# Kernel tuning notes

Measured on AMD Instinct MI355X. Metric: run time of the kernel, lower is better.

## Reference

```python
import jax, jax.numpy as jnp
import numpy as np

BN_EPS = 1e-5


def _bn_relu(h, gamma, beta):
    # BatchNorm1d in training mode: batch stats over the edge dimension, biased var
    mu = jnp.mean(h, axis=0)
    var = jnp.mean((h - mu) ** 2, axis=0)
    return jax.nn.relu((h - mu) * jax.lax.rsqrt(var + BN_EPS) * gamma + beta)


def setup_inputs() -> dict:
    key = jax.random.key(0)
    ks = jax.random.split(key, 6)
    B, P, C, O, K = 8, 2048, 64, 64, 20  # clouds, points/cloud, in_ch, out_ch, knn
    N = B * P
    x = jax.random.normal(ks[0], (N, C), jnp.float32)
    pos = jax.random.normal(ks[1], (N, 3), jnp.float32)
    batch = jnp.repeat(jnp.arange(B, dtype=jnp.int32), P)  # sorted cloud ids
    # MLP params: Linear(2C, O) -> BN -> ReLU -> Linear(O, O) -> BN -> ReLU
    W1 = jax.random.normal(ks[2], (O, 2 * C), jnp.float32) / np.sqrt(2 * C)
    b1 = jnp.zeros((O,), jnp.float32)
    g1 = jnp.ones((O,), jnp.float32)
    beta1 = jnp.zeros((O,), jnp.float32)
    W2 = jax.random.normal(ks[3], (O, O), jnp.float32) / np.sqrt(O)
    b2 = jnp.zeros((O,), jnp.float32)
    g2 = jnp.ones((O,), jnp.float32)
    beta2 = jnp.zeros((O,), jnp.float32)
    return {"x": x, "pos": pos, "batch": batch, "W1": W1, "b1": b1, "g1": g1,
            "beta1": beta1, "W2": W2, "b2": b2, "g2": g2, "beta2": beta2, "k": K}


def reference(x, pos, batch, W1, b1, g1, beta1, W2, b2, g2, beta2, k):
    N, C = x.shape
    B = int(batch[-1]) + 1          # equal-size, sorted clouds
    P = N // B
    p = pos.reshape(B, P, -1)
    # knn_graph (loop=False): brute-force squared distances per cloud
    sq = jnp.sum(p * p, axis=-1)                      # [B,P]
    d2 = sq[:, :, None] + sq[:, None, :] - 2.0 * jnp.einsum('bpd,bqd->bpq', p, p)
    d2 = jnp.where(jnp.eye(P, dtype=bool)[None], jnp.inf, d2)  # no self-loops
    _, nbr = jax.lax.top_k(-d2, k)                    # [B,P,k] neighbor idx in cloud
    offset = (jnp.arange(B, dtype=nbr.dtype) * P)[:, None, None]
    # torch_cluster knn_graph flow='source_to_target': row = neighbor j, col = center i
    row = (nbr + offset).reshape(-1)                  # [N*k]
    col = jnp.repeat(jnp.arange(N, dtype=row.dtype), k)
    x_r = x[row]
    edge_features = jnp.concatenate([x_r, x[col] - x_r], axis=1)  # [N*k, 2C]
    h = _bn_relu(edge_features @ W1.T + b1, g1, beta1)
    h = _bn_relu(h @ W2.T + b2, g2, beta2)
    out = jax.ops.segment_max(h, row, num_segments=N)
    # torch_scatter scatter(reduce='max') leaves empty rows at 0
    return jnp.where(jnp.isneginf(out), 0.0, out)
```

## Files before the change

### kernel.cpp

```cpp
#include <hip/hip_runtime.h>

constexpr int BATCH = 8;
constexpr int PPC   = 2048;
constexpr int NPT   = BATCH * PPC;
constexpr int OCH   = 64;
constexpr int KNN_K = 20;
constexpr int NEDGE = NPT * KNN_K;
constexpr int REVCAP = 128;
constexpr int OVCAP  = 8192;
constexpr int QCAP   = 48;
constexpr int NPART  = 32;

typedef short short8 __attribute__((ext_vector_type(8)));
typedef float float4v __attribute__((ext_vector_type(4)));

__device__ __forceinline__ int xcd_swizzle(int b, int nper) {
  return (b & 7) * nper + (b >> 3);
}

__device__ __forceinline__ unsigned short bfr(float f) {
  unsigned u = __float_as_uint(f);
  return (unsigned short)((u + 0x7FFFu + ((u >> 16) & 1u)) >> 16);
}
__device__ __forceinline__ short8 pack8(float4 a, float4 b) {
  short8 r;
  r[0] = (short)bfr(a.x); r[1] = (short)bfr(a.y);
  r[2] = (short)bfr(a.z); r[3] = (short)bfr(a.w);
  r[4] = (short)bfr(b.x); r[5] = (short)bfr(b.y);
  r[6] = (short)bfr(b.z); r[7] = (short)bfr(b.w);
  return r;
}
__device__ __forceinline__ unsigned umed3(unsigned a, unsigned b, unsigned c) {
  unsigned d;
  asm("v_med3_u32 %0, %1, %2, %3" : "=v"(d) : "v"(a), "v"(b), "v"(c));
  return d;
}

__global__ __launch_bounds__(256) void knn_kernel(const float* __restrict__ pos,
                                                  int* __restrict__ nbr,
                                                  int* __restrict__ cnt,
                                                  int* __restrict__ ovf_cnt,
                                                  int* __restrict__ ovf,
                                                  int* __restrict__ rev) {
  __shared__ float4 cps[8 * 257];
  __shared__ unsigned long long qk[16][QCAP];
  __shared__ int qn[16];
  const int t  = threadIdx.x;
  const int pl = t >> 4;
  const int s  = t & 15;
  const int lane = t & 63;
  const int eb = xcd_swizzle(blockIdx.x, NPT / 16 / 8);
  const int i  = eb * 16 + pl;
  const int cbase = i & ~(PPC - 1);

  for (int u = t; u < PPC; u += 256) {
    int j = cbase + u;
    float ax = pos[3 * j], ay = pos[3 * j + 1], az = pos[3 * j + 2];
    cps[(u >> 8) * 257 + (u & 255)] = make_float4(ax, ay, az, ax * ax + ay * ay + az * az);
  }
  if (t < 16) qn[t] = 0;
  __syncthreads();

  const int il = i - cbase;
  const float4 me = cps[(il >> 8) * 257 + (il & 255)];
  const float px = me.x, py = me.y, pz = me.z, sqi = me.w;
  const int jbase = s * 128;
  const float4* __restrict__ cp = &cps[(s >> 1) * 257 + (s & 1) * 128];

  unsigned kd[3];
  kd[0] = kd[1] = kd[2] = 0xFFFFFFFFu;
  for (int u = 0; u < 128; ++u) {
    float4 c = cp[u];
    float pr = fmaf(-px, c.x, fmaf(-py, c.y, fmaf(-pz, c.z, fmaf(0.5f, c.w, 1000.f))));
    unsigned ck = __float_as_uint(pr);
    ck = (jbase + u == il) ? 0xFFFFFFFFu : ck;
    kd[2] = umed3(kd[1], kd[2], ck);
    kd[1] = umed3(kd[0], kd[1], ck);
    kd[0] = kd[0] < ck ? kd[0] : ck;
  }

  unsigned T = 0xFFFFFFFFu;
  int cum = 0;
  const int grp = lane & 48;
#pragma unroll
  for (int r = 0; r < KNN_K; ++r) {
    unsigned w = kd[0];
#pragma unroll
    for (int m = 1; m < 16; m <<= 1) {
      unsigned o = (unsigned)__shfl_xor((int)w, m, 16);
      w = o < w ? o : w;
    }
    bool pop = (kd[0] == w);
    unsigned long long bal = __ballot(pop);
    int mcount = __popc((int)((bal >> grp) & 0xFFFFull));
    if (cum < KNN_K) T = w;
    cum += mcount;
    if (pop) { kd[0] = kd[1]; kd[1] = kd[2]; kd[2] = 0xFFFFFFFFu; }
  }
  const unsigned Tq = T + 16;

  for (int u = 0; u < 128; ++u) {
    float4 c = cp[u];
    float pr = fmaf(-px, c.x, fmaf(-py, c.y, fmaf(-pz, c.z, fmaf(0.5f, c.w, 1000.f))));
    unsigned ck = __float_as_uint(pr);
    ck = (jbase + u == il) ? 0xFFFFFFFFu : ck;
    if (ck <= Tq) {
      float d2 = sqi + c.w - 2.0f * (px * c.x + py * c.y + pz * c.z);
      d2 = d2 > 0.f ? d2 : 0.f;
      int slot = atomicAdd(&qn[pl], 1);
      if (slot < QCAP)
        qk[pl][slot] = ((unsigned long long)__float_as_uint(d2) << 32) | (unsigned)(jbase + u);
    }
  }
  __syncthreads();

  int n = qn[pl]; n = n < QCAP ? n : QCAP;
  for (int base = 0; base < n; base += 16) {
    int e = base + s;
    if (e < n) {
      unsigned long long mk = qk[pl][e];
      int rank = 0;
      for (int o = 0; o < n; ++o) rank += (qk[pl][o] < mk) ? 1 : 0;
      if (rank < KNN_K) {
        int j = cbase + (int)(mk & 0xFFFFFFFFull);
        int eid = i * KNN_K + rank;
        nbr[eid] = j;
        int slot = atomicAdd(&cnt[j], 1);
        if (slot < REVCAP) rev[j * REVCAP + slot] = i;
        else { int ov = atomicAdd(ovf_cnt, 1); if (ov < OVCAP) ovf[ov] = eid; }
      }
    }
  }
}

__global__ __launch_bounds__(256) void node_gemm(const float* __restrict__ x,
                                                 const float* __restrict__ W1,
                                                 float* __restrict__ yv,
                                                 float* __restrict__ zv) {
  __shared__ float wa[64][65];
  __shared__ float wb[64][65];
  __shared__ float xs[16][64];
  const int t = threadIdx.x;
  for (int m = t; m < 8192; m += 256) {
    int o = m >> 7, c2 = m & 127;
    float w = W1[m];
    if (c2 < 64) wa[c2][o] = w; else wb[c2 - 64][o] = w;
  }
  for (int m = t; m < 1024; m += 256)
    xs[m >> 6][m & 63] = x[(size_t)blockIdx.x * 1024 + m];
  __syncthreads();
  const int g = t >> 6, o = t & 63;
  float accA[4] = {0, 0, 0, 0}, accB[4] = {0, 0, 0, 0};
#pragma unroll 4
  for (int c = 0; c < 64; ++c) {
    float w_a = wa[c][o], w_b = wb[c][o];
#pragma unroll
    for (int q = 0; q < 4; ++q) {
      float xv = xs[g * 4 + q][c];
      accA[q] = fmaf(xv, w_a, accA[q]);
      accB[q] = fmaf(xv, w_b, accB[q]);
    }
  }
#pragma unroll
  for (int q = 0; q < 4; ++q) {
    size_t n = (size_t)blockIdx.x * 16 + g * 4 + q;
    yv[n * 64 + o] = accA[q] - accB[q];
    zv[n * 64 + o] = accB[q];
  }
}

__global__ __launch_bounds__(256) void bn1_stats(const int* __restrict__ nbr,
                                                 const float4* __restrict__ yv4,
                                                 const float4* __restrict__ zv4,
                                                 const float* __restrict__ b1,
                                                 float* __restrict__ bn1p) {
  const int t  = threadIdx.x;
  const int c4 = t & 15;
  const int lane = t & 63;
  const int eb = xcd_swizzle(blockIdx.x, NPT / 16 / 8);
  const int i  = eb * 16 + (t >> 4);
  const float4 bo = reinterpret_cast<const float4*>(b1)[c4];
  float4 z = zv4[(size_t)i * 16 + c4];
  float4 zb = make_float4(z.x + bo.x, z.y + bo.y, z.z + bo.z, z.w + bo.w);
  int jA = nbr[i * KNN_K + c4];
  int jB = nbr[i * KNN_K + 16 + (c4 & 3)];
  float4 s1 = make_float4(0, 0, 0, 0), s2 = make_float4(0, 0, 0, 0);
#pragma unroll
  for (int q = 0; q < 16; ++q) {
    int j = __shfl(jA, (lane & 48) + q);
    float4 y = yv4[(size_t)j * 16 + c4];
    float sx = y.x + zb.x, sy = y.y + zb.y, sz = y.z + zb.z, sw = y.w + zb.w;
    s1.x += sx; s1.y += sy; s1.z += sz; s1.w += sw;
    s2.x += sx * sx; s2.y += sy * sy; s2.z += sz * sz; s2.w += sw * sw;
  }
#pragma unroll
  for (int q = 0; q < 4; ++q) {
    int j = __shfl(jB, (lane & 48) + q);
    float4 y = yv4[(size_t)j * 16 + c4];
    float sx = y.x + zb.x, sy = y.y + zb.y, sz = y.z + zb.z, sw = y.w + zb.w;
    s1.x += sx; s1.y += sy; s1.z += sz; s1.w += sw;
    s2.x += sx * sx; s2.y += sy * sy; s2.z += sz * sz; s2.w += sw * sw;
  }
  s1.x += __shfl_xor(s1.x, 16); s1.y += __shfl_xor(s1.y, 16);
  s1.z += __shfl_xor(s1.z, 16); s1.w += __shfl_xor(s1.w, 16);
  s2.x += __shfl_xor(s2.x, 16); s2.y += __shfl_xor(s2.y, 16);
  s2.z += __shfl_xor(s2.z, 16); s2.w += __shfl_xor(s2.w, 16);
  s1.x += __shfl_xor(s1.x, 32); s1.y += __shfl_xor(s1.y, 32);
  s1.z += __shfl_xor(s1.z, 32); s1.w += __shfl_xor(s1.w, 32);
  s2.x += __shfl_xor(s2.x, 32); s2.y += __shfl_xor(s2.y, 32);
  s2.z += __shfl_xor(s2.z, 32); s2.w += __shfl_xor(s2.w, 32);
  __shared__ float ss[2][64];
  if (t < 128) { ss[0][t & 63] = 0.f; }
  __syncthreads();
  if ((t & 48) == 0) {
    atomicAdd(&ss[0][c4 * 4 + 0], s1.x); atomicAdd(&ss[0][c4 * 4 + 1], s1.y);
    atomicAdd(&ss[0][c4 * 4 + 2], s1.z); atomicAdd(&ss[0][c4 * 4 + 3], s1.w);
    atomicAdd(&ss[1][c4 * 4 + 0], s2.x); atomicAdd(&ss[1][c4 * 4 + 1], s2.y);
    atomicAdd(&ss[1][c4 * 4 + 2], s2.z); atomicAdd(&ss[1][c4 * 4 + 3], s2.w);
  }
  __syncthreads();
  const int pb = (blockIdx.x & (NPART - 1)) * 128;
  if (t < 64)       atomicAdd(&bn1p[pb + t], ss[0][t]);
  else if (t < 128) atomicAdd(&bn1p[pb + 64 + (t - 64)], ss[1][t - 64]);
}

__global__ __launch_bounds__(256) void scale_yz(
    const float4* __restrict__ yv4, const float4* __restrict__ zv4,
    const float* __restrict__ bn1p, const float* __restrict__ g1,
    const float* __restrict__ beta1, const float* __restrict__ b1,
    float4* __restrict__ ys4, float4* __restrict__ zs4) {
  __shared__ float red[128];
  const int t = threadIdx.x;
  if (t < 128) {
    float v = 0.f;
#pragma unroll
    for (int k = 0; k < NPART; ++k) v += bn1p[k * 128 + t];
    red[t] = v;
  }
  __syncthreads();
  const int idx = blockIdx.x * 256 + t;
  const int c4 = idx & 15;
  constexpr float invE = 1.0f / NEDGE;
  float a[4], c[4];
#pragma unroll
  for (int q = 0; q < 4; ++q) {
    int ch = c4 * 4 + q;
    float mu  = red[ch] * invE;
    float var = red[64 + ch] * invE - mu * mu;
    float av  = g1[ch] * rsqrtf(var + 1e-5f);
    a[q] = av;
    c[q] = fmaf(b1[ch], av, beta1[ch] - mu * av);
  }
  float4 y = yv4[idx];
  float4 z = zv4[idx];
  ys4[idx] = make_float4(y.x * a[0], y.y * a[1], y.z * a[2], y.w * a[3]);
  zs4[idx] = make_float4(fmaf(z.x, a[0], c[0]), fmaf(z.y, a[1], c[1]),
                         fmaf(z.z, a[2], c[2]), fmaf(z.w, a[3], c[3]));
}

__global__ __launch_bounds__(256) void gemm2_row(
    const float4* __restrict__ ys4, const float4* __restrict__ zs4,
    const float* __restrict__ W2, const float* __restrict__ b2,
    const int* __restrict__ cnt, const int* __restrict__ rev,
    float* __restrict__ bn2p, float* __restrict__ mmax,
    float* __restrict__ mmin) {
  __shared__ float ss[2][64];
  const int t = threadIdx.x, lane = t & 63;
  const int col = lane & 15, quad = lane >> 4;
  const int eb = xcd_swizzle(blockIdx.x, NPT / 16 / 8);
  const int wid = eb * 4 + (t >> 6);

  short8 bf0[4], bf1[4];
  const float4* __restrict__ W2v = (const float4*)W2;
#pragma unroll
  for (int nt = 0; nt < 4; ++nt) {
    int row = nt * 16 + col;
    float4 wa = W2v[row * 16 + quad * 2];
    float4 wb = W2v[row * 16 + quad * 2 + 1];
    float4 wc = W2v[row * 16 + 8 + quad * 2];
    float4 wd = W2v[row * 16 + 8 + quad * 2 + 1];
    bf0[nt] = pack8(wa, wb);
    bf1[nt] = pack8(wc, wd);
  }
  float b2r[4];
#pragma unroll
  for (int nt = 0; nt < 4; ++nt) b2r[nt] = b2[nt * 16 + col];

  int4 cq = *reinterpret_cast<const int4*>(&cnt[wid * 4]);
  int nA[4] = {cq.x, cq.y, cq.z, cq.w};
#pragma unroll
  for (int q = 0; q < 4; ++q) nA[q] = nA[q] < REVCAP ? nA[q] : REVCAP;

  float s1[4] = {0, 0, 0, 0}, s2[4] = {0, 0, 0, 0};
  int rv0 = rev[(size_t)(wid * 4) * REVCAP + lane];
  int rv1 = (nA[0] > 64) ? rev[(size_t)(wid * 4) * REVCAP + 64 + lane] : 0;
  float4 ya = ys4[(size_t)(wid * 4) * 16 + quad * 2];
  float4 yb = ys4[(size_t)(wid * 4) * 16 + quad * 2 + 1];
  float4 yc = ys4[(size_t)(wid * 4) * 16 + 8 + quad * 2];
  float4 yd = ys4[(size_t)(wid * 4) * 16 + 8 + quad * 2 + 1];

#pragma unroll
  for (int rr = 0; rr < 4; ++rr) {
    const int row = wid * 4 + rr;
    const int n = nA[rr];
    int nrv0 = 0, nrv1 = 0;
    float4 nya, nyb, nyc, nyd;
    if (rr < 3) {
      const int nrow = row + 1;
      nrv0 = rev[(size_t)nrow * REVCAP + lane];
      nrv1 = (nA[rr + 1] > 64) ? rev[(size_t)nrow * REVCAP + 64 + lane] : 0;
      nya = ys4[(size_t)nrow * 16 + quad * 2];
      nyb = ys4[(size_t)nrow * 16 + quad * 2 + 1];
      nyc = ys4[(size_t)nrow * 16 + 8 + quad * 2];
      nyd = ys4[(size_t)nrow * 16 + 8 + quad * 2 + 1];
    }
    float mx[4], mn[4];
#pragma unroll
    for (int nt = 0; nt < 4; ++nt) { mx[nt] = -1e30f; mn[nt] = 1e30f; }

    auto tile_body = [&](int tbase, float4 za, float4 zb, float4 zc, float4 zd) {
      float h[16];
      h[0]  = ya.x + za.x; h[1]  = ya.y + za.y; h[2]  = ya.z + za.z; h[3]  = ya.w + za.w;
      h[4]  = yb.x + zb.x; h[5]  = yb.y + zb.y; h[6]  = yb.z + zb.z; h[7]  = yb.w + zb.w;
      h[8]  = yc.x + zc.x; h[9]  = yc.y + zc.y; h[10] = yc.z + zc.z; h[11] = yc.w + zc.w;
      h[12] = yd.x + zd.x; h[13] = yd.y + zd.y; h[14] = yd.z + zd.z; h[15] = yd.w + zd.w;
      short8 af0, af1;
#pragma unroll
      for (int q = 0; q < 8; ++q) {
        float u0 = h[q]     > 0.f ? h[q]     : 0.f;
        float u1 = h[8 + q] > 0.f ? h[8 + q] : 0.f;
        af0[q] = (short)bfr(u0);
        af1[q] = (short)bfr(u1);
      }
      float4v acc[4];
#pragma unroll
      for (int nt = 0; nt < 4; ++nt) {
        acc[nt] = (float4v){0.f, 0.f, 0.f, 0.f};
        acc[nt] = __builtin_amdgcn_mfma_f32_16x16x32_bf16(af0, bf0[nt], acc[nt], 0, 0, 0);
        acc[nt] = __builtin_amdgcn_mfma_f32_16x16x32_bf16(af1, bf1[nt], acc[nt], 0, 0, 0);
      }
#pragma unroll
      for (int r = 0; r < 4; ++r) {
        bool v = (tbase + quad * 4 + r) < n;
#pragma unroll
        for (int nt = 0; nt < 4; ++nt) {
          float val = acc[nt][r] + b2r[nt];
          if (v) {
            s1[nt] += val; s2[nt] += val * val;
            mx[nt] = val > mx[nt] ? val : mx[nt];
            mn[nt] = val < mn[nt] ? val : mn[nt];
          }
        }
      }
    };

    int icA = __shfl(rv0, col);       icA = (col < n) ? icA : 0;
    int icB = __shfl(rv0, 16 + col);  icB = (16 + col < n) ? icB : 0;
    float4 zAa = zs4[(size_t)icA * 16 + quad * 2];
    float4 zAb = zs4[(size_t)icA * 16 + quad * 2 + 1];
    float4 zAc = zs4[(size_t)icA * 16 + 8 + quad * 2];
    float4 zAd = zs4[(size_t)icA * 16 + 8 + quad * 2 + 1];
    float4 zBa = zs4[(size_t)icB * 16 + quad * 2];
    float4 zBb = zs4[(size_t)icB * 16 + quad * 2 + 1];
    float4 zBc = zs4[(size_t)icB * 16 + 8 + quad * 2];
    float4 zBd = zs4[(size_t)icB * 16 + 8 + quad * 2 + 1];
    tile_body(0, zAa, zAb, zAc, zAd);
    if (n > 16) tile_body(16, zBa, zBb, zBc, zBd);
    for (int ti = 2; ti * 16 < n; ++ti) {
      int gi = ti * 16 + col;
      int v0 = __shfl(rv0, gi & 63);
      int v1 = __shfl(rv1, gi & 63);
      int ic = (gi < 64) ? v0 : v1;
      ic = (gi < n) ? ic : 0;
      float4 za = zs4[(size_t)ic * 16 + quad * 2];
      float4 zb = zs4[(size_t)ic * 16 + quad * 2 + 1];
      float4 zc = zs4[(size_t)ic * 16 + 8 + quad * 2];
      float4 zd = zs4[(size_t)ic * 16 + 8 + quad * 2 + 1];
      tile_body(ti * 16, za, zb, zc, zd);
    }
#pragma unroll
    for (int nt = 0; nt < 4; ++nt) {
      mx[nt] = fmaxf(mx[nt], __shfl_xor(mx[nt], 16));
      mx[nt] = fmaxf(mx[nt], __shfl_xor(mx[nt], 32));
      mn[nt] = fminf(mn[nt], __shfl_xor(mn[nt], 16));
      mn[nt] = fminf(mn[nt], __shfl_xor(mn[nt], 32));
    }
    if (quad == 0) {
#pragma unroll
      for (int nt = 0; nt < 4; ++nt) {
        mmax[(size_t)row * 64 + nt * 16 + col] = mx[nt];
        mmin[(size_t)row * 64 + nt * 16 + col] = mn[nt];
      }
    }
    rv0 = nrv0; rv1 = nrv1;
    ya = nya; yb = nyb; yc = nyc; yd = nyd;
  }
  if (t < 128) ss[t >> 6][t & 63] = 0.f;
  __syncthreads();
#pragma unroll
  for (int nt = 0; nt < 4; ++nt) {
    s1[nt] += __shfl_xor(s1[nt], 16);
    s1[nt] += __shfl_xor(s1[nt], 32);
    s2[nt] += __shfl_xor(s2[nt], 16);
    s2[nt] += __shfl_xor(s2[nt], 32);
  }
  if (quad == 0) {
#pragma unroll
    for (int nt = 0; nt < 4; ++nt) {
      atomicAdd(&ss[0][nt * 16 + col], s1[nt]);
      atomicAdd(&ss[1][nt * 16 + col], s2[nt]);
    }
  }
  __syncthreads();
  const int pb = (blockIdx.x & (NPART - 1)) * 128;
  if (t < 64)       atomicAdd(&bn2p[pb + t], ss[0][t]);
  else if (t < 128) atomicAdd(&bn2p[pb + 64 + (t - 64)], ss[1][t - 64]);
}

__global__ __launch_bounds__(256) void finalize_out(
    const float* __restrict__ bn2p, const float* __restrict__ g2,
    const float* __restrict__ beta2, const int* __restrict__ cnt,
    const float* __restrict__ mmax, const float* __restrict__ mmin,
    const int* __restrict__ ovf_cnt, const int* __restrict__ ovf,
    const int* __restrict__ nbr, const float* __restrict__ ys,
    const float* __restrict__ zs, const float* __restrict__ W2,
    const float* __restrict__ b2, float* __restrict__ outp) {
  __shared__ float red[128];
  const int t = threadIdx.x;
  if (t < 128) {
    float v = 0.f;
#pragma unroll
    for (int k = 0; k < NPART; ++k) v += bn2p[k * 128 + t];
    red[t] = v;
  }
  __syncthreads();
  const int idx = blockIdx.x * 256 + t;
  const int row = idx >> 6, ch = idx & 63;
  constexpr float invE = 1.0f / NEDGE;
  float mu  = red[ch] * invE;
  float var = red[64 + ch] * invE - mu * mu;
  float a2  = g2[ch] * rsqrtf(var + 1e-5f);
  float c2  = beta2[ch] - mu * a2;
  float h = (a2 >= 0.f) ? mmax[idx] : mmin[idx];
  int ov = ovf_cnt[0]; ov = ov > OVCAP ? OVCAP : ov;
  for (int u = 0; u < ov; ++u) {
    int e = ovf[u];
    if (nbr[e] == row) {
      int ic = e / KNN_K;
      float accv = 0.f;
      for (int k = 0; k < 64; ++k) {
        float hh = ys[(size_t)row * 64 + k] + zs[(size_t)ic * 64 + k];
        hh = hh > 0.f ? hh : 0.f;
        accv = fmaf(hh, W2[ch * 64 + k], accv);
      }
      float v = accv + b2[ch];
      if (a2 >= 0.f) h = v > h ? v : h; else h = v < h ? v : h;
    }
  }
  float o = (cnt[row] > 0) ? fmaf(h, a2, c2) : 0.0f;
  outp[idx] = o > 0.f ? o : 0.f;
}

extern "C" void kernel_launch(void* const* d_in, const int* in_sizes, int n_in,
                              void* d_out, int out_size, void* d_ws, size_t ws_size,
                              hipStream_t stream) {
  (void)in_sizes; (void)n_in; (void)out_size; (void)ws_size;
  const float* x     = (const float*)d_in[0];
  const float* pos   = (const float*)d_in[1];
  const float* W1    = (const float*)d_in[3];
  const float* b1    = (const float*)d_in[4];
  const float* g1    = (const float*)d_in[5];
  const float* beta1 = (const float*)d_in[6];
  const float* W2    = (const float*)d_in[7];
  const float* b2    = (const float*)d_in[8];
  const float* g2    = (const float*)d_in[9];
  const float* beta2 = (const float*)d_in[10];
  float* outp = (float*)d_out;

  char* w = (char*)d_ws;
  int*   nbr     = (int*)w;
  float* yv      = (float*)(w + 1310720);
  float* zv      = (float*)(w + 5505024);
  int*   cnt     = (int*)(w + 9700352);
  int*   ovf_cnt = (int*)(w + 9765888);
  int*   ovf     = (int*)(w + 9765952);
  int*   rev     = (int*)(w + 9798720);
  float* mmax    = (float*)(w + 18187328);
  float* mmin    = (float*)(w + 22381632);
  float* ys      = (float*)(w + 26575936);
  float* zs      = (float*)(w + 30770240);
  float* bn1p    = (float*)(w + 34964544);
  float* bn2p    = (float*)(w + 34980928);

  hipMemsetAsync(cnt, 0, 65536 + 64, stream);
  hipMemsetAsync(bn1p, 0, 32768, stream);

  knn_kernel<<<NPT / 16, 256, 0, stream>>>(pos, nbr, cnt, ovf_cnt, ovf, rev);
  node_gemm<<<NPT / 16, 256, 0, stream>>>(x, W1, yv, zv);
  bn1_stats<<<NPT / 16, 256, 0, stream>>>(nbr, (const float4*)yv, (const float4*)zv, b1, bn1p);
  scale_yz<<<NPT * 16 / 256, 256, 0, stream>>>(
      (const float4*)yv, (const float4*)zv, bn1p, g1, beta1, b1,
      (float4*)ys, (float4*)zs);
  gemm2_row<<<NPT / 16, 256, 0, stream>>>(
      (const float4*)ys, (const float4*)zs, W2, b2,
      cnt, rev, bn2p, mmax, mmin);
  finalize_out<<<NPT * 64 / 256, 256, 0, stream>>>(
      bn2p, g2, beta2, cnt, mmax, mmin, ovf_cnt, ovf, nbr,
      ys, zs, W2, b2, outp);
}
```

Measured before the change: 188.1 us.

## Fuse BN1 statistics into kNN kernel and drop per-candidate self-exclusion

Moves node_gemm ahead of the kNN launch and folds the bn1_stats kernel into the kNN kernel. Selected neighbour indices are broadcast into a per-thread register array and used to accumulate the BN1 sums directly, so nbr is no longer re-read and one launch disappears. The self-exclusion select is removed from the top-3 scan; instead the threshold search keeps K+1 candidates and the self point is skipped during candidate collection. The risks are higher register pressure from the dynamically indexed res array, which may spill to scratch, and a somewhat larger candidate queue.

```diff
diff --git a/kernel.cpp b/kernel.cpp
--- a/kernel.cpp
+++ b/kernel.cpp
@@ -37,14 +37,19 @@
 }
 
 __global__ __launch_bounds__(256) void knn_kernel(const float* __restrict__ pos,
+                                                  const float4* __restrict__ yv4,
+                                                  const float4* __restrict__ zv4,
+                                                  const float* __restrict__ b1,
                                                   int* __restrict__ nbr,
                                                   int* __restrict__ cnt,
                                                   int* __restrict__ ovf_cnt,
                                                   int* __restrict__ ovf,
-                                                  int* __restrict__ rev) {
+                                                  int* __restrict__ rev,
+                                                  float* __restrict__ bn1p) {
   __shared__ float4 cps[8 * 257];
   __shared__ unsigned long long qk[16][QCAP];
   __shared__ int qn[16];
+  __shared__ float ss[2][64];
   const int t  = threadIdx.x;
   const int pl = t >> 4;
   const int s  = t & 15;
@@ -73,7 +78,6 @@
     float4 c = cp[u];
     float pr = fmaf(-px, c.x, fmaf(-py, c.y, fmaf(-pz, c.z, fmaf(0.5f, c.w, 1000.f))));
     unsigned ck = __float_as_uint(pr);
-    ck = (jbase + u == il) ? 0xFFFFFFFFu : ck;
     kd[2] = umed3(kd[1], kd[2], ck);
     kd[1] = umed3(kd[0], kd[1], ck);
     kd[0] = kd[0] < ck ? kd[0] : ck;
@@ -83,7 +87,7 @@
   int cum = 0;
   const int grp = lane & 48;
 #pragma unroll
-  for (int r = 0; r < KNN_K; ++r) {
+  for (int r = 0; r < KNN_K + 1; ++r) {
     unsigned w = kd[0];
 #pragma unroll
     for (int m = 1; m < 16; m <<= 1) {
@@ -93,7 +97,7 @@
     bool pop = (kd[0] == w);
     unsigned long long bal = __ballot(pop);
     int mcount = __popc((int)((bal >> grp) & 0xFFFFull));
-    if (cum < KNN_K) T = w;
+    if (cum < KNN_K + 1) T = w;
     cum += mcount;
     if (pop) { kd[0] = kd[1]; kd[1] = kd[2]; kd[2] = 0xFFFFFFFFu; }
   }
@@ -103,8 +107,7 @@
     float4 c = cp[u];
     float pr = fmaf(-px, c.x, fmaf(-py, c.y, fmaf(-pz, c.z, fmaf(0.5f, c.w, 1000.f))));
     unsigned ck = __float_as_uint(pr);
-    ck = (jbase + u == il) ? 0xFFFFFFFFu : ck;
-    if (ck <= Tq) {
+    if (ck <= Tq && jbase + u != il) {
       float d2 = sqi + c.w - 2.0f * (px * c.x + py * c.y + pz * c.z);
       d2 = d2 > 0.f ? d2 : 0.f;
       int slot = atomicAdd(&qn[pl], 1);
@@ -115,14 +118,18 @@
   __syncthreads();
 
   int n = qn[pl]; n = n < QCAP ? n : QCAP;
+  int res[KNN_K];
   for (int base = 0; base < n; base += 16) {
     int e = base + s;
+    int rnk = -1, jloc = 0;
     if (e < n) {
       unsigned long long mk = qk[pl][e];
       int rank = 0;
       for (int o = 0; o < n; ++o) rank += (qk[pl][o] < mk) ? 1 : 0;
+      jloc = (int)(mk & 0xFFFFFFFFull);
       if (rank < KNN_K) {
-        int j = cbase + (int)(mk & 0xFFFFFFFFull);
+        rnk = rank;
+        int j = cbase + jloc;
         int eid = i * KNN_K + rank;
         nbr[eid] = j;
         int slot = atomicAdd(&cnt[j], 1);
@@ -130,7 +137,48 @@
         else { int ov = atomicAdd(ovf_cnt, 1); if (ov < OVCAP) ovf[ov] = eid; }
       }
     }
-  }
+    unsigned long long bal = __ballot(rnk >= 0);
+    unsigned short msk = (unsigned short)((bal >> grp) & 0xFFFFull);
+    while (msk) {
+      int src = __ffs((int)msk) - 1;
+      int r  = __shfl(rnk,  grp + src);
+      int jl = __shfl(jloc, grp + src);
+      res[r] = jl;
+      msk &= msk - 1;
+    }
+  }
+
+  const float4 bo = reinterpret_cast<const float4*>(b1)[s];
+  float4 z = zv4[(size_t)i * 16 + s];
+  float4 zb = make_float4(z.x + bo.x, z.y + bo.y, z.z + bo.z, z.w + bo.w);
+  float4 s1 = make_float4(0, 0, 0, 0), s2 = make_float4(0, 0, 0, 0);
+#pragma unroll
+  for (int q = 0; q < KNN_K; ++q) {
+    float4 y = yv4[(size_t)(cbase + res[q]) * 16 + s];
+    float sx = y.x + zb.x, sy = y.y + zb.y, sz = y.z + zb.z, sw = y.w + zb.w;
+    s1.x += sx; s1.y += sy; s1.z += sz; s1.w += sw;
+    s2.x += sx * sx; s2.y += sy * sy; s2.z += sz * sz; s2.w += sw * sw;
+  }
+  s1.x += __shfl_xor(s1.x, 16); s1.y += __shfl_xor(s1.y, 16);
+  s1.z += __shfl_xor(s1.z, 16); s1.w += __shfl_xor(s1.w, 16);
+  s2.x += __shfl_xor(s2.x, 16); s2.y += __shfl_xor(s2.y, 16);
+  s2.z += __shfl_xor(s2.z, 16); s2.w += __shfl_xor(s2.w, 16);
+  s1.x += __shfl_xor(s1.x, 32); s1.y += __shfl_xor(s1.y, 32);
+  s1.z += __shfl_xor(s1.z, 32); s1.w += __shfl_xor(s1.w, 32);
+  s2.x += __shfl_xor(s2.x, 32); s2.y += __shfl_xor(s2.y, 32);
+  s2.z += __shfl_xor(s2.z, 32); s2.w += __shfl_xor(s2.w, 32);
+  if (t < 128) ss[t >> 6][t & 63] = 0.f;
+  __syncthreads();
+  if ((t & 48) == 0) {
+    atomicAdd(&ss[0][s * 4 + 0], s1.x); atomicAdd(&ss[0][s * 4 + 1], s1.y);
+    atomicAdd(&ss[0][s * 4 + 2], s1.z); atomicAdd(&ss[0][s * 4 + 3], s1.w);
+    atomicAdd(&ss[1][s * 4 + 0], s2.x); atomicAdd(&ss[1][s * 4 + 1], s2.y);
+    atomicAdd(&ss[1][s * 4 + 2], s2.z); atomicAdd(&ss[1][s * 4 + 3], s2.w);
+  }
+  __syncthreads();
+  const int pb = (blockIdx.x & (NPART - 1)) * 128;
+  if (t < 64)       atomicAdd(&bn1p[pb + t], ss[0][t]);
+  else if (t < 128) atomicAdd(&bn1p[pb + 64 + (t - 64)], ss[1][t - 64]);
 }
 
 __global__ __launch_bounds__(256) void node_gemm(const float* __restrict__ x,
@@ -167,61 +215,6 @@
     yv[n * 64 + o] = accA[q] - accB[q];
     zv[n * 64 + o] = accB[q];
   }
-}
-
-__global__ __launch_bounds__(256) void bn1_stats(const int* __restrict__ nbr,
-                                                 const float4* __restrict__ yv4,
-                                                 const float4* __restrict__ zv4,
-                                                 const float* __restrict__ b1,
-                                                 float* __restrict__ bn1p) {
-  const int t  = threadIdx.x;
-  const int c4 = t & 15;
-  const int lane = t & 63;
-  const int eb = xcd_swizzle(blockIdx.x, NPT / 16 / 8);
-  const int i  = eb * 16 + (t >> 4);
-  const float4 bo = reinterpret_cast<const float4*>(b1)[c4];
-  float4 z = zv4[(size_t)i * 16 + c4];
-  float4 zb = make_float4(z.x + bo.x, z.y + bo.y, z.z + bo.z, z.w + bo.w);
-  int jA = nbr[i * KNN_K + c4];
-  int jB = nbr[i * KNN_K + 16 + (c4 & 3)];
-  float4 s1 = make_float4(0, 0, 0, 0), s2 = make_float4(0, 0, 0, 0);
-#pragma unroll
-  for (int q = 0; q < 16; ++q) {
-    int j = __shfl(jA, (lane & 48) + q);
-    float4 y = yv4[(size_t)j * 16 + c4];
-    float sx = y.x + zb.x, sy = y.y + zb.y, sz = y.z + zb.z, sw = y.w + zb.w;
-    s1.x += sx; s1.y += sy; s1.z += sz; s1.w += sw;
-    s2.x += sx * sx; s2.y += sy * sy; s2.z += sz * sz; s2.w += sw * sw;
-  }
-#pragma unroll
-  for (int q = 0; q < 4; ++q) {
-    int j = __shfl(jB, (lane & 48) + q);
-    float4 y = yv4[(size_t)j * 16 + c4];
-    float sx = y.x + zb.x, sy = y.y + zb.y, sz = y.z + zb.z, sw = y.w + zb.w;
-    s1.x += sx; s1.y += sy; s1.z += sz; s1.w += sw;
-    s2.x += sx * sx; s2.y += sy * sy; s2.z += sz * sz; s2.w += sw * sw;
-  }
-  s1.x += __shfl_xor(s1.x, 16); s1.y += __shfl_xor(s1.y, 16);
-  s1.z += __shfl_xor(s1.z, 16); s1.w += __shfl_xor(s1.w, 16);
-  s2.x += __shfl_xor(s2.x, 16); s2.y += __shfl_xor(s2.y, 16);
-  s2.z += __shfl_xor(s2.z, 16); s2.w += __shfl_xor(s2.w, 16);
-  s1.x += __shfl_xor(s1.x, 32); s1.y += __shfl_xor(s1.y, 32);
-  s1.z += __shfl_xor(s1.z, 32); s1.w += __shfl_xor(s1.w, 32);
-  s2.x += __shfl_xor(s2.x, 32); s2.y += __shfl_xor(s2.y, 32);
-  s2.z += __shfl_xor(s2.z, 32); s2.w += __shfl_xor(s2.w, 32);
-  __shared__ float ss[2][64];
-  if (t < 128) { ss[0][t & 63] = 0.f; }
-  __syncthreads();
-  if ((t & 48) == 0) {
-    atomicAdd(&ss[0][c4 * 4 + 0], s1.x); atomicAdd(&ss[0][c4 * 4 + 1], s1.y);
-    atomicAdd(&ss[0][c4 * 4 + 2], s1.z); atomicAdd(&ss[0][c4 * 4 + 3], s1.w);
-    atomicAdd(&ss[1][c4 * 4 + 0], s2.x); atomicAdd(&ss[1][c4 * 4 + 1], s2.y);
-    atomicAdd(&ss[1][c4 * 4 + 2], s2.z); atomicAdd(&ss[1][c4 * 4 + 3], s2.w);
-  }
-  __syncthreads();
-  const int pb = (blockIdx.x & (NPART - 1)) * 128;
-  if (t < 64)       atomicAdd(&bn1p[pb + t], ss[0][t]);
-  else if (t < 128) atomicAdd(&bn1p[pb + 64 + (t - 64)], ss[1][t - 64]);
 }
 
 __global__ __launch_bounds__(256) void scale_yz(
@@ -495,9 +488,9 @@
   hipMemsetAsync(cnt, 0, 65536 + 64, stream);
   hipMemsetAsync(bn1p, 0, 32768, stream);
 
-  knn_kernel<<<NPT / 16, 256, 0, stream>>>(pos, nbr, cnt, ovf_cnt, ovf, rev);
   node_gemm<<<NPT / 16, 256, 0, stream>>>(x, W1, yv, zv);
-  bn1_stats<<<NPT / 16, 256, 0, stream>>>(nbr, (const float4*)yv, (const float4*)zv, b1, bn1p);
+  knn_kernel<<<NPT / 16, 256, 0, stream>>>(pos, (const float4*)yv, (const float4*)zv,
+                                           b1, nbr, cnt, ovf_cnt, ovf, rev, bn1p);
   scale_yz<<<NPT * 16 / 256, 256, 0, stream>>>(
       (const float4*)yv, (const float4*)zv, bn1p, g1, beta1, b1,
       (float4*)ys, (float4*)zs);
```

New measurement: 189.5 us. No clear change (+0.8%).
